# Performance work log

Measured on AMD Instinct MI355X. Metric: run time of the kernel, lower is better.

Reference implementation:

```python
import jax, jax.numpy as jnp
import numpy as np

K = 1024          # num_embeddings
D = 64            # embedding_dim
EPS = 0.05        # entropic regularization epsilon
DUAL_STEPS = 10
DUAL_LR = 0.5
TEMP = 0.5        # hist_temperature
OT_W = 1.0
CC = 0.25         # commitment cost


def _norm_prob(p):
    p = jnp.clip(p, 1e-12)
    return p / p.sum()


def _dual_obj(phi, src_w, tgt_w, cost):
    src_w = _norm_prob(src_w)
    tgt_w = _norm_prob(tgt_w)
    log_tgt = jnp.log(jnp.clip(tgt_w, 1e-12))[None, :]          # [1, K]
    lse = jax.scipy.special.logsumexp(log_tgt + (-cost + phi[None, :]) / EPS, axis=1)  # [K]
    return jnp.sum(src_w * (-EPS * lse)) + jnp.sum(tgt_w * phi)


def _dual_ot_loss(src_w, tgt_w, cost):
    src_d = jax.lax.stop_gradient(src_w)
    tgt_d = jax.lax.stop_gradient(tgt_w)
    cost_d = jax.lax.stop_gradient(cost)
    grad_phi = jax.grad(_dual_obj)
    def body(_, phi):
        return phi + DUAL_LR * grad_phi(phi, src_d, tgt_d, cost_d)
    phi = jax.lax.fori_loop(0, DUAL_STEPS, body, jnp.zeros_like(tgt_d))
    return _dual_obj(jax.lax.stop_gradient(phi), src_w, tgt_w, cost)


def _gaussian_target():
    idx = jnp.arange(K, dtype=jnp.float32)
    mean = (K - 1) / 2.0
    std = K / 6.0
    t = jnp.exp(-0.5 * ((idx - mean) / std) ** 2)
    return t / jnp.clip(t.sum(), 1e-12)


def _forward(inputs, codebook):
    B, C, H, W = inputs.shape
    x_bhwc = jnp.transpose(inputs, (0, 2, 3, 1))                 # [B,H,W,C]
    flat = x_bhwc.reshape(-1, C)                                  # [N, D]
    # squared-distance matrix [N, K]
    d = (jnp.sum(flat * flat, axis=1, keepdims=True)
         + jnp.sum(codebook * codebook, axis=1)
         - 2.0 * flat @ codebook.T)
    idx = jnp.argmin(d, axis=1)                                   # [N]
    enc = jax.nn.one_hot(idx, K, dtype=jnp.float32)               # [N, K]
    # power normalize (one-hot power = sqrt(1/K) < 1, so a no-op, but faithful)
    power = jnp.sqrt(jnp.mean(enc * enc))
    enc = jnp.where(power > 1.0, enc / power, enc)
    clean_q = enc @ codebook                                      # [N, D]
    noisy_q = clean_q                                             # channel=None -> zero noise
    # training losses
    hard_hist = jnp.mean(enc, axis=0)                             # [K]
    soft = jax.nn.softmax(-d / TEMP, axis=1)                      # [N, K]
    soft_hist = jnp.mean(soft, axis=0)
    # value = hard_hist, gradient flows via soft_hist (straight-through hist)
    cw = _norm_prob(hard_hist + soft_hist - jax.lax.stop_gradient(soft_hist))
    target = _gaussian_target()
    support = jnp.arange(K, dtype=jnp.float32)
    cost = jnp.abs(support[:, None] - support[None, :])           # cdist(p=2) on 1-d support
    ot_loss = OT_W * _dual_ot_loss(cw, target, cost)
    codebook_loss = jnp.mean((clean_q - jax.lax.stop_gradient(flat)) ** 2)
    commit_loss = jnp.mean((jax.lax.stop_gradient(clean_q) - flat) ** 2)
    loss = codebook_loss + CC * commit_loss + ot_loss
    # straight-through quantized output
    nq = noisy_q.reshape(B, H, W, C)
    quantized = x_bhwc + jax.lax.stop_gradient(nq - x_bhwc)
    quantized = jnp.transpose(quantized, (0, 3, 1, 2))            # [B,C,H,W]
    avg = jnp.mean(enc, axis=0)
    perplexity = jnp.exp(-jnp.sum(avg * jnp.log(avg + 1e-10)))
    return quantized, loss, perplexity


def setup_inputs() -> dict:
    key = jax.random.key(0)
    k1, k2 = jax.random.split(key)
    inputs = jax.random.normal(k1, (32, D, 32, 32), dtype=jnp.float32)
    codebook = jax.random.uniform(k2, (K, D), minval=-1.0 / K, maxval=1.0 / K, dtype=jnp.float32)
    return {"inputs": inputs, "codebook": codebook}


def reference(inputs, codebook):
    return _forward(inputs, codebook)
```

## Files before the change

kernel.cpp:

```cpp
#include <hip/hip_runtime.h>
#include <math.h>

#define NPTS 32768
#define KCB  1024
#define DIM  64
#define HW   1024
#define CHW  65536
#define RWIN 2

typedef short  bf16x8 __attribute__((ext_vector_type(8)));
typedef float  f32x16 __attribute__((ext_vector_type(16)));

__device__ __forceinline__ unsigned short f2b_rne(float f) {
  unsigned u = __float_as_uint(f);
  unsigned r = 0x7FFFu + ((u >> 16) & 1u);
  return (unsigned short)((u + r) >> 16);
}

__device__ __forceinline__ float block_sum(float v, float* scratch) {
  #pragma unroll
  for (int o = 32; o > 0; o >>= 1) v += __shfl_down(v, o, 64);
  int wid  = threadIdx.x >> 6;
  int lane = threadIdx.x & 63;
  __syncthreads();
  if (lane == 0) scratch[wid] = v;
  __syncthreads();
  float s = 0.f;
  int nw = blockDim.x >> 6;
  for (int w = 0; w < nw; ++w) s += scratch[w];
  return s;
}

__global__ __launch_bounds__(64) void k_cvt(const float* __restrict__ cb,
                                            float4* __restrict__ cbf,
                                            float* __restrict__ cnorm) {
  int c = blockIdx.x * 64 + threadIdx.x;
  const float4* row4 = (const float4*)(cb + c * DIM);
  float4 r[16];
  #pragma unroll
  for (int i = 0; i < 16; ++i) r[i] = row4[i];
  float s = 0.f;
  #pragma unroll
  for (int i = 0; i < 16; ++i) {
    s = fmaf(r[i].x, r[i].x, s); s = fmaf(r[i].y, r[i].y, s);
    s = fmaf(r[i].z, r[i].z, s); s = fmaf(r[i].w, r[i].w, s);
  }
  cnorm[c] = s;
  int ch = c >> 6, nt = (c >> 5) & 1, n = c & 31;
  int base = ch * 1024 + nt * 256 + n;
  #pragma unroll
  for (int o = 0; o < 8; ++o) {
    float f[8] = {r[2*o].x, r[2*o].y, r[2*o].z, r[2*o].w,
                  r[2*o+1].x, r[2*o+1].y, r[2*o+1].z, r[2*o+1].w};
    unsigned hu[4], lu[4];
    #pragma unroll
    for (int j = 0; j < 4; ++j) {
      unsigned short h0 = f2b_rne(f[2*j]),   h1 = f2b_rne(f[2*j+1]);
      float hf0 = __uint_as_float((unsigned)h0 << 16);
      float hf1 = __uint_as_float((unsigned)h1 << 16);
      unsigned short l0 = f2b_rne(f[2*j] - hf0), l1 = f2b_rne(f[2*j+1] - hf1);
      hu[j] = (unsigned)h0 | ((unsigned)h1 << 16);
      lu[j] = (unsigned)l0 | ((unsigned)l1 << 16);
    }
    int pos = base + (o >> 1) * 64 + (o & 1) * 32;
    uint4 hv = {hu[0], hu[1], hu[2], hu[3]};
    uint4 lv = {lu[0], lu[1], lu[2], lu[3]};
    cbf[pos]       = *(float4*)&hv;
    cbf[pos + 512] = *(float4*)&lv;
  }
}

__global__ __launch_bounds__(256, 2) void k_dist(const float* __restrict__ x,
                                                 const float* __restrict__ cb,
                                                 const float4* __restrict__ cbf,
                                                 const float* __restrict__ cnorm,
                                                 int* __restrict__ hist,
                                                 float* __restrict__ msep,
                                                 float* __restrict__ out) {
  __shared__ unsigned short lph[64][72], lpl[64][72];
  __shared__ short bbuf[2][8192];
  __shared__ float s_cn[KCB];
  __shared__ float s_sx[64], s_part[4][64];
  __shared__ unsigned long long s_pk[64][2];
  __shared__ int   s_bd[64];
  __shared__ float scratch[4];

  int tid = threadIdx.x;
  int t   = blockIdx.x;
  int n0  = t * 64;
  int b   = n0 >> 10;
  int hw0 = n0 & 1023;

  *(float4*)&s_cn[tid * 4] = *(const float4*)(cnorm + tid * 4);

  {
    int p = tid & 63, q4 = tid >> 6;
    const float* xb = x + b * CHW + hw0 + p;
    float s = 0.f;
    unsigned short hb[16], lb[16];
    #pragma unroll
    for (int i = 0; i < 16; ++i) {
      int c = q4 * 16 + i;
      float f = xb[c * HW];
      s = fmaf(f, f, s);
      unsigned short h = f2b_rne(f);
      float hf = __uint_as_float(((unsigned)h) << 16);
      hb[i] = h;
      lb[i] = f2b_rne(f - hf);
    }
    s_part[q4][p] = s;
    #pragma unroll
    for (int j = 0; j < 8; ++j) {
      *(unsigned*)&lph[p][q4 * 16 + 2 * j] = (unsigned)hb[2*j] | ((unsigned)hb[2*j+1] << 16);
      *(unsigned*)&lpl[p][q4 * 16 + 2 * j] = (unsigned)lb[2*j] | ((unsigned)lb[2*j+1] << 16);
    }
  }
  float4 pf[4];
  #pragma unroll
  for (int j = 0; j < 4; ++j) pf[j] = cbf[tid + 256 * j];
  __syncthreads();
  if (tid < 64)
    s_sx[tid] = ((s_part[0][tid] + s_part[1][tid]) + s_part[2][tid]) + s_part[3][tid];
  __syncthreads();

  int w = tid >> 6, l = tid & 63;
  int wm = w >> 1, wn = w & 1;
  int u = l >> 5, n = l & 31;

  bf16x8 ah[4], al[4];
  {
    int pt = wm * 32 + n;
    #pragma unroll
    for (int s = 0; s < 4; ++s) {
      ah[s] = *(const bf16x8*)&lph[pt][(2 * s + u) * 8];
      al[s] = *(const bf16x8*)&lpl[pt][(2 * s + u) * 8];
    }
  }
  float sxr[16];
  #pragma unroll
  for (int r = 0; r < 16; ++r)
    sxr[r] = s_sx[wm * 32 + (r & 3) + 8 * (r >> 2) + 4 * u];

  float best[16]; int bidx[16];
  #pragma unroll
  for (int r = 0; r < 16; ++r) { best[r] = 3.4e38f; bidx[r] = 0; }

  int bofs = wn * 256 + u * 32 + n;

  for (int ch = 0; ch < 16; ++ch) {
    int bb = ch & 1;
    #pragma unroll
    for (int j = 0; j < 4; ++j)
      *(float4*)&bbuf[bb][(tid + 256 * j) * 8] = pf[j];
    if (ch < 15) {
      #pragma unroll
      for (int j = 0; j < 4; ++j)
        pf[j] = cbf[(ch + 1) * 1024 + tid + 256 * j];
    }
    __builtin_amdgcn_s_waitcnt(0xc07f);
    __builtin_amdgcn_s_barrier();

    f32x16 acc;
    #pragma unroll
    for (int r = 0; r < 16; ++r) acc[r] = 0.f;
    #pragma unroll
    for (int s = 0; s < 4; ++s) {
      bf16x8 bh = *(const bf16x8*)&bbuf[bb][(bofs + s * 64) * 8];
      bf16x8 bl = *(const bf16x8*)&bbuf[bb][(bofs + s * 64 + 512) * 8];
      acc = __builtin_amdgcn_mfma_f32_32x32x16_bf16(ah[s], bh, acc, 0, 0, 0);
      acc = __builtin_amdgcn_mfma_f32_32x32x16_bf16(ah[s], bl, acc, 0, 0, 0);
      acc = __builtin_amdgcn_mfma_f32_32x32x16_bf16(al[s], bh, acc, 0, 0, 0);
    }
    float cnv = s_cn[ch * 64 + wn * 32 + n];
    int   kk  = ch * 64 + wn * 32 + n;
    #pragma unroll
    for (int r = 0; r < 16; ++r) {
      float dist = (sxr[r] + cnv) - 2.0f * acc[r];
      if (dist < best[r]) { best[r] = dist; bidx[r] = kk; }
    }
  }

  #pragma unroll
  for (int r = 0; r < 16; ++r) {
    unsigned long long p =
        ((unsigned long long)__float_as_uint(best[r]) << 32) | (unsigned)bidx[r];
    #pragma unroll
    for (int m = 1; m < 32; m <<= 1) {
      unsigned long long o = __shfl_xor(p, m, 64);
      p = (o < p) ? o : p;
    }
    if (n == 0)
      s_pk[wm * 32 + (r & 3) + 8 * (r >> 2) + 4 * u][wn] = p;
  }
  __syncthreads();
  if (tid < 64) {
    unsigned long long a = s_pk[tid][0], c2 = s_pk[tid][1];
    unsigned long long mn = (c2 < a) ? c2 : a;
    int bd = (int)(mn & 0xffffffffull);
    s_bd[tid] = bd;
    atomicAdd(&hist[bd], 1);
  }
  __syncthreads();

  float se = 0.f;
  {
    int p = tid & 63, cg = tid >> 6;
    int bd = s_bd[p];
    const float* crow = cb + bd * DIM;
    const float* xp = x + b * CHW + hw0 + p;
    float* ob = out + b * CHW + hw0 + p;
    #pragma unroll 4
    for (int i = 0; i < 16; ++i) {
      int c = cg * 16 + i;
      float xv   = xp[c * HW];
      float diff = crow[c] - xv;
      se += diff * diff;
      ob[c * HW] = xv + diff;
    }
  }
  float tot = block_sum(se, scratch);
  if (tid == 0) msep[t] = tot;
}

__global__ __launch_bounds__(256) void k_ot(const int* __restrict__ hist,
                                            const float* __restrict__ msep,
                                            float* __restrict__ out) {
  __shared__ __align__(16) float s_lt[KCB + 8], s_src[KCB + 8],
                                 s_phi[KCB + 8], s_lse[KCB + 8];
  __shared__ float scratch[4];
  int tid = threadIdx.x;
  int i0  = tid * 4;
  int sl0 = i0 + 4;

  float msetot = block_sum(msep[tid] + msep[tid + 256], scratch);

  int4 hi4 = *(const int4*)(hist + i0);
  int  hi[4] = {hi4.x, hi4.y, hi4.z, hi4.w};
  float tj[4], hj[4];
  #pragma unroll
  for (int j = 0; j < 4; ++j) {
    float fi = (float)(i0 + j);
    float zz = (fi - 511.5f) / (1024.0f / 6.0f);
    tj[j] = expf(-0.5f * zz * zz);
    hj[j] = (float)hi[j] * (1.0f / 32768.0f);
  }
  float St = block_sum(tj[0] + tj[1] + tj[2] + tj[3], scratch);
  float tgt[4], ltw[4];
  float l2 = 0.f;
  #pragma unroll
  for (int j = 0; j < 4; ++j) { tgt[j] = fmaxf(tj[j] / fmaxf(St, 1e-12f), 1e-12f); l2 += tgt[j]; }
  float St2 = block_sum(l2, scratch);
  #pragma unroll
  for (int j = 0; j < 4; ++j) { tgt[j] = tgt[j] / St2; ltw[j] = logf(fmaxf(tgt[j], 1e-12f)); }

  float m1[4], srcw[4];
  float l3 = 0.f;
  #pragma unroll
  for (int j = 0; j < 4; ++j) { m1[j] = fmaxf(hj[j], 1e-12f); l3 += m1[j]; }
  float S1 = block_sum(l3, scratch);
  float l4 = 0.f;
  #pragma unroll
  for (int j = 0; j < 4; ++j) { srcw[j] = fmaxf(m1[j] / S1, 1e-12f); l4 += srcw[j]; }
  float S2 = block_sum(l4, scratch);
  float l5 = 0.f;
  #pragma unroll
  for (int j = 0; j < 4; ++j) { srcw[j] = srcw[j] / S2; l5 += hj[j] * logf(hj[j] + 1e-10f); }
  float ent = block_sum(l5, scratch);

  *(float4*)&s_lt[sl0]  = *(float4*)ltw;
  *(float4*)&s_src[sl0] = *(float4*)srcw;
  *(float4*)&s_phi[sl0] = make_float4(0.f, 0.f, 0.f, 0.f);
  *(float4*)&s_lse[sl0] = make_float4(0.f, 0.f, 0.f, 0.f);
  if (tid == 0) {
    #pragma unroll
    for (int p = 0; p < 4; ++p) {
      s_lt[p] = -100.f; s_src[p] = 0.f; s_phi[p] = 0.f; s_lse[p] = 0.f;
      s_lt[KCB+4+p] = -100.f; s_src[KCB+4+p] = 0.f; s_phi[KCB+4+p] = 0.f; s_lse[KCB+4+p] = 0.f;
    }
  }
  __syncthreads();

  float ws[12];
  #pragma unroll
  for (int m = 0; m < 3; ++m) *(float4*)&ws[m*4] = *(float4*)&s_src[i0 + m*4];

  float phi[4] = {0.f, 0.f, 0.f, 0.f};
  float lse[4];
  for (int it = 0; it <= 10; ++it) {
    float wl[12], wp[12];
    #pragma unroll
    for (int m = 0; m < 3; ++m) {
      *(float4*)&wl[m*4] = *(float4*)&s_lt[i0 + m*4];
      *(float4*)&wp[m*4] = *(float4*)&s_phi[i0 + m*4];
    }
    #pragma unroll
    for (int j = 0; j < 4; ++j) {
      float mx = -3.0e38f;
      float vv[5];
      #pragma unroll
      for (int qq = 0; qq < 5; ++qq) {
        int m = j + qq + 2;
        float a = wl[m] + (wp[m] - fabsf((float)(qq - 2))) * 20.0f;
        vv[qq] = a;
        mx = fmaxf(mx, a);
      }
      float ssum = 0.f;
      #pragma unroll
      for (int qq = 0; qq < 5; ++qq) ssum += expf(vv[qq] - mx);
      lse[j] = mx + logf(ssum);
    }
    *(float4*)&s_lse[sl0] = *(float4*)lse;
    __syncthreads();
    if (it == 10) break;

    float we[12];
    #pragma unroll
    for (int m = 0; m < 3; ++m) *(float4*)&we[m*4] = *(float4*)&s_lse[i0 + m*4];
    #pragma unroll
    for (int j = 0; j < 4; ++j) {
      float basej = ltw[j] + phi[j] * 20.0f;
      float cs = 0.f;
      #pragma unroll
      for (int qq = 0; qq < 5; ++qq) {
        int m = j + qq + 2;
        float a = basej - fabsf((float)(qq - 2)) * 20.0f;
        cs += ws[m] * expf(a - we[m]);
      }
      phi[j] += 0.5f * (tgt[j] - cs);
    }
    *(float4*)&s_phi[sl0] = *(float4*)phi;
    __syncthreads();
  }

  float lo = 0.f;
  #pragma unroll
  for (int j = 0; j < 4; ++j) lo += srcw[j] * (-0.05f * lse[j]) + tgt[j] * phi[j];
  float ot = block_sum(lo, scratch);

  if (tid == 0) {
    out[2097152] = 1.25f * (msetot * (1.0f / 2097152.0f)) + ot;
    out[2097153] = expf(-ent);
  }
}

extern "C" void kernel_launch(void* const* d_in, const int* in_sizes, int n_in,
                              void* d_out, int out_size, void* d_ws, size_t ws_size,
                              hipStream_t stream) {
  const float* x  = (const float*)d_in[0];
  const float* cb = (const float*)d_in[1];
  float* out = (float*)d_out;

  float4* cbf  = (float4*)d_ws;
  float*  cnorm = (float*)((char*)d_ws + 262144);
  int*    hist  = (int*)((char*)d_ws + 266240);
  float*  msep  = (float*)((char*)d_ws + 270336);

  hipMemsetAsync(hist, 0, 4096, stream);
  k_cvt<<<16, 64, 0, stream>>>(cb, cbf, cnorm);
  k_dist<<<512, 256, 0, stream>>>(x, cb, cbf, cnorm, hist, msep, out);
  k_ot<<<1, 256, 0, stream>>>(hist, msep, out);
}
```

Measured before the change: 131.5 us.

## Fuse OT solve into distance kernel via last-block pattern and restructure MFMA tiling

Drops the memset and the separate single-block OT kernel. k_cvt now zeroes the histogram and counters, and the last k_dist block to finish, found with an atomic counter, runs the dual OT iterations. k_dist now uses 128-thread blocks of 32 points. Each wave covers half the codebook and loads codebook fragments straight from global memory into registers instead of double-buffering through LDS, and x is cached in LDS for the output pass. The aim is to cut launch overhead and LDS barriers, at the cost of re-reading codebook tiles per block and a serialized OT tail inside the last block.

```diff
diff --git a/kernel.cpp b/kernel.cpp
--- a/kernel.cpp
+++ b/kernel.cpp
@@ -6,7 +6,6 @@
 #define DIM  64
 #define HW   1024
 #define CHW  65536
-#define RWIN 2
 
 typedef short  bf16x8 __attribute__((ext_vector_type(8)));
 typedef float  f32x16 __attribute__((ext_vector_type(16)));
@@ -20,21 +19,25 @@
 __device__ __forceinline__ float block_sum(float v, float* scratch) {
   #pragma unroll
   for (int o = 32; o > 0; o >>= 1) v += __shfl_down(v, o, 64);
-  int wid  = threadIdx.x >> 6;
-  int lane = threadIdx.x & 63;
+  int wid = threadIdx.x >> 6, lane = threadIdx.x & 63;
   __syncthreads();
   if (lane == 0) scratch[wid] = v;
   __syncthreads();
   float s = 0.f;
   int nw = blockDim.x >> 6;
-  for (int w = 0; w < nw; ++w) s += scratch[w];
+  for (int w2 = 0; w2 < nw; ++w2) s += scratch[w2];
   return s;
 }
 
 __global__ __launch_bounds__(64) void k_cvt(const float* __restrict__ cb,
                                             float4* __restrict__ cbf,
-                                            float* __restrict__ cnorm) {
+                                            float* __restrict__ cnorm,
+                                            int* __restrict__ hist,
+                                            int* __restrict__ done,
+                                            float* __restrict__ mseacc) {
   int c = blockIdx.x * 64 + threadIdx.x;
+  hist[c] = 0;
+  if (c == 0) { *done = 0; *mseacc = 0.f; }
   const float4* row4 = (const float4*)(cb + c * DIM);
   float4 r[16];
   #pragma unroll
@@ -70,130 +73,132 @@
   }
 }
 
-__global__ __launch_bounds__(256, 2) void k_dist(const float* __restrict__ x,
+__global__ __launch_bounds__(128, 2) void k_dist(const float* __restrict__ x,
                                                  const float* __restrict__ cb,
                                                  const float4* __restrict__ cbf,
                                                  const float* __restrict__ cnorm,
                                                  int* __restrict__ hist,
-                                                 float* __restrict__ msep,
+                                                 int* __restrict__ done,
+                                                 float* __restrict__ mseacc,
                                                  float* __restrict__ out) {
-  __shared__ unsigned short lph[64][72], lpl[64][72];
-  __shared__ short bbuf[2][8192];
-  __shared__ float s_cn[KCB];
-  __shared__ float s_sx[64], s_part[4][64];
-  __shared__ unsigned long long s_pk[64][2];
-  __shared__ int   s_bd[64];
-  __shared__ float scratch[4];
+  __shared__ float4 s_af[2][4][64];
+  __shared__ float  lpf[64][32];
+  __shared__ float  s_part[4][32];
+  __shared__ float  s_sx[32];
+  __shared__ unsigned long long s_pk[32][2];
+  __shared__ int    s_bd[32];
+  __shared__ float  scratch[2];
+  __shared__ int    s_last;
+  __shared__ __align__(16) float s_lt[KCB + 8], s_src[KCB + 8],
+                                 s_phi[KCB + 8], s_lse[KCB + 8];
 
   int tid = threadIdx.x;
   int t   = blockIdx.x;
-  int n0  = t * 64;
+  int n0  = t * 32;
   int b   = n0 >> 10;
   int hw0 = n0 & 1023;
-
-  *(float4*)&s_cn[tid * 4] = *(const float4*)(cnorm + tid * 4);
+  int p   = tid & 31, g = tid >> 5;
 
   {
-    int p = tid & 63, q4 = tid >> 6;
     const float* xb = x + b * CHW + hw0 + p;
     float s = 0.f;
     unsigned short hb[16], lb[16];
     #pragma unroll
     for (int i = 0; i < 16; ++i) {
-      int c = q4 * 16 + i;
+      int c = g * 16 + i;
       float f = xb[c * HW];
       s = fmaf(f, f, s);
+      lpf[c][p] = f;
       unsigned short h = f2b_rne(f);
       float hf = __uint_as_float(((unsigned)h) << 16);
       hb[i] = h;
       lb[i] = f2b_rne(f - hf);
     }
-    s_part[q4][p] = s;
-    #pragma unroll
-    for (int j = 0; j < 8; ++j) {
-      *(unsigned*)&lph[p][q4 * 16 + 2 * j] = (unsigned)hb[2*j] | ((unsigned)hb[2*j+1] << 16);
-      *(unsigned*)&lpl[p][q4 * 16 + 2 * j] = (unsigned)lb[2*j] | ((unsigned)lb[2*j+1] << 16);
-    }
-  }
-  float4 pf[4];
-  #pragma unroll
-  for (int j = 0; j < 4; ++j) pf[j] = cbf[tid + 256 * j];
-  __syncthreads();
-  if (tid < 64)
+    s_part[g][p] = s;
+    unsigned hu0[4], hu1[4], lu0[4], lu1[4];
+    #pragma unroll
+    for (int j = 0; j < 4; ++j) {
+      hu0[j] = (unsigned)hb[2*j]     | ((unsigned)hb[2*j+1] << 16);
+      hu1[j] = (unsigned)hb[8+2*j]   | ((unsigned)hb[8+2*j+1] << 16);
+      lu0[j] = (unsigned)lb[2*j]     | ((unsigned)lb[2*j+1] << 16);
+      lu1[j] = (unsigned)lb[8+2*j]   | ((unsigned)lb[8+2*j+1] << 16);
+    }
+    uint4 a0 = {hu0[0],hu0[1],hu0[2],hu0[3]}, a1 = {hu1[0],hu1[1],hu1[2],hu1[3]};
+    uint4 c0 = {lu0[0],lu0[1],lu0[2],lu0[3]}, c1 = {lu1[0],lu1[1],lu1[2],lu1[3]};
+    s_af[0][g][p]      = *(float4*)&a0;
+    s_af[0][g][32 + p] = *(float4*)&a1;
+    s_af[1][g][p]      = *(float4*)&c0;
+    s_af[1][g][32 + p] = *(float4*)&c1;
+  }
+  __syncthreads();
+  if (tid < 32)
     s_sx[tid] = ((s_part[0][tid] + s_part[1][tid]) + s_part[2][tid]) + s_part[3][tid];
   __syncthreads();
 
-  int w = tid >> 6, l = tid & 63;
-  int wm = w >> 1, wn = w & 1;
+  int w = tid >> 6;
+  int l = tid & 63;
   int u = l >> 5, n = l & 31;
 
   bf16x8 ah[4], al[4];
-  {
-    int pt = wm * 32 + n;
-    #pragma unroll
-    for (int s = 0; s < 4; ++s) {
-      ah[s] = *(const bf16x8*)&lph[pt][(2 * s + u) * 8];
-      al[s] = *(const bf16x8*)&lpl[pt][(2 * s + u) * 8];
-    }
+  #pragma unroll
+  for (int s4 = 0; s4 < 4; ++s4) {
+    ah[s4] = *(bf16x8*)&s_af[0][s4][l];
+    al[s4] = *(bf16x8*)&s_af[1][s4][l];
   }
   float sxr[16];
   #pragma unroll
-  for (int r = 0; r < 16; ++r)
-    sxr[r] = s_sx[wm * 32 + (r & 3) + 8 * (r >> 2) + 4 * u];
+  for (int r = 0; r < 16; ++r) sxr[r] = s_sx[(r & 3) + 8 * (r >> 2) + 4 * u];
 
   float best[16]; int bidx[16];
   #pragma unroll
   for (int r = 0; r < 16; ++r) { best[r] = 3.4e38f; bidx[r] = 0; }
 
-  int bofs = wn * 256 + u * 32 + n;
-
-  for (int ch = 0; ch < 16; ++ch) {
-    int bb = ch & 1;
-    #pragma unroll
-    for (int j = 0; j < 4; ++j)
-      *(float4*)&bbuf[bb][(tid + 256 * j) * 8] = pf[j];
-    if (ch < 15) {
-      #pragma unroll
-      for (int j = 0; j < 4; ++j)
-        pf[j] = cbf[(ch + 1) * 1024 + tid + 256 * j];
-    }
-    __builtin_amdgcn_s_waitcnt(0xc07f);
-    __builtin_amdgcn_s_barrier();
-
-    f32x16 acc;
-    #pragma unroll
-    for (int r = 0; r < 16; ++r) acc[r] = 0.f;
-    #pragma unroll
-    for (int s = 0; s < 4; ++s) {
-      bf16x8 bh = *(const bf16x8*)&bbuf[bb][(bofs + s * 64) * 8];
-      bf16x8 bl = *(const bf16x8*)&bbuf[bb][(bofs + s * 64 + 512) * 8];
-      acc = __builtin_amdgcn_mfma_f32_32x32x16_bf16(ah[s], bh, acc, 0, 0, 0);
-      acc = __builtin_amdgcn_mfma_f32_32x32x16_bf16(ah[s], bl, acc, 0, 0, 0);
-      acc = __builtin_amdgcn_mfma_f32_32x32x16_bf16(al[s], bh, acc, 0, 0, 0);
-    }
-    float cnv = s_cn[ch * 64 + wn * 32 + n];
-    int   kk  = ch * 64 + wn * 32 + n;
+  #pragma unroll 1
+  for (int c8 = 0; c8 < 8; ++c8) {
+    int ch = w * 8 + c8;
+    const float4* bp = cbf + ch * 1024 + l;
+    float4 bh[8], bl[8];
+    #pragma unroll
+    for (int q2 = 0; q2 < 8; ++q2) {
+      bh[q2] = bp[q2 * 64];
+      bl[q2] = bp[q2 * 64 + 512];
+    }
+    float cn0 = cnorm[ch * 64 + n];
+    float cn1 = cnorm[ch * 64 + 32 + n];
+    f32x16 a0, a1;
+    #pragma unroll
+    for (int r = 0; r < 16; ++r) { a0[r] = 0.f; a1[r] = 0.f; }
+    #pragma unroll
+    for (int s4 = 0; s4 < 4; ++s4) {
+      a0 = __builtin_amdgcn_mfma_f32_32x32x16_bf16(ah[s4], *(bf16x8*)&bh[s4],     a0, 0, 0, 0);
+      a1 = __builtin_amdgcn_mfma_f32_32x32x16_bf16(ah[s4], *(bf16x8*)&bh[4 + s4], a1, 0, 0, 0);
+      a0 = __builtin_amdgcn_mfma_f32_32x32x16_bf16(ah[s4], *(bf16x8*)&bl[s4],     a0, 0, 0, 0);
+      a1 = __builtin_amdgcn_mfma_f32_32x32x16_bf16(ah[s4], *(bf16x8*)&bl[4 + s4], a1, 0, 0, 0);
+      a0 = __builtin_amdgcn_mfma_f32_32x32x16_bf16(al[s4], *(bf16x8*)&bh[s4],     a0, 0, 0, 0);
+      a1 = __builtin_amdgcn_mfma_f32_32x32x16_bf16(al[s4], *(bf16x8*)&bh[4 + s4], a1, 0, 0, 0);
+    }
     #pragma unroll
     for (int r = 0; r < 16; ++r) {
-      float dist = (sxr[r] + cnv) - 2.0f * acc[r];
-      if (dist < best[r]) { best[r] = dist; bidx[r] = kk; }
+      float d0 = (sxr[r] + cn0) - 2.0f * a0[r];
+      if (d0 < best[r]) { best[r] = d0; bidx[r] = ch * 64 + n; }
+      float d1 = (sxr[r] + cn1) - 2.0f * a1[r];
+      if (d1 < best[r]) { best[r] = d1; bidx[r] = ch * 64 + 32 + n; }
     }
   }
 
   #pragma unroll
   for (int r = 0; r < 16; ++r) {
-    unsigned long long p =
+    unsigned long long pk =
         ((unsigned long long)__float_as_uint(best[r]) << 32) | (unsigned)bidx[r];
     #pragma unroll
     for (int m = 1; m < 32; m <<= 1) {
-      unsigned long long o = __shfl_xor(p, m, 64);
-      p = (o < p) ? o : p;
-    }
-    if (n == 0)
-      s_pk[wm * 32 + (r & 3) + 8 * (r >> 2) + 4 * u][wn] = p;
-  }
-  __syncthreads();
-  if (tid < 64) {
+      unsigned long long o = __shfl_xor(pk, m, 64);
+      pk = (o < pk) ? o : pk;
+    }
+    if (n == 0) s_pk[(r & 3) + 8 * (r >> 2) + 4 * u][w] = pk;
+  }
+  __syncthreads();
+  if (tid < 32) {
     unsigned long long a = s_pk[tid][0], c2 = s_pk[tid][1];
     unsigned long long mn = (c2 < a) ? c2 : a;
     int bd = (int)(mn & 0xffffffffull);
@@ -204,137 +209,144 @@
 
   float se = 0.f;
   {
-    int p = tid & 63, cg = tid >> 6;
     int bd = s_bd[p];
     const float* crow = cb + bd * DIM;
-    const float* xp = x + b * CHW + hw0 + p;
-    float* ob = out + b * CHW + hw0 + p;
+    float* op = out + b * CHW + hw0 + p;
     #pragma unroll 4
     for (int i = 0; i < 16; ++i) {
-      int c = cg * 16 + i;
-      float xv   = xp[c * HW];
+      int c = g * 16 + i;
+      float xv   = lpf[c][p];
       float diff = crow[c] - xv;
       se += diff * diff;
-      ob[c * HW] = xv + diff;
+      op[c * HW] = xv + diff;
     }
   }
   float tot = block_sum(se, scratch);
-  if (tid == 0) msep[t] = tot;
-}
-
-__global__ __launch_bounds__(256) void k_ot(const int* __restrict__ hist,
-                                            const float* __restrict__ msep,
-                                            float* __restrict__ out) {
-  __shared__ __align__(16) float s_lt[KCB + 8], s_src[KCB + 8],
-                                 s_phi[KCB + 8], s_lse[KCB + 8];
-  __shared__ float scratch[4];
-  int tid = threadIdx.x;
-  int i0  = tid * 4;
-  int sl0 = i0 + 4;
-
-  float msetot = block_sum(msep[tid] + msep[tid + 256], scratch);
-
-  int4 hi4 = *(const int4*)(hist + i0);
-  int  hi[4] = {hi4.x, hi4.y, hi4.z, hi4.w};
-  float tj[4], hj[4];
-  #pragma unroll
-  for (int j = 0; j < 4; ++j) {
+  if (tid == 0) {
+    atomicAdd(mseacc, tot);
+    __threadfence();
+    int old = atomicAdd(done, 1);
+    s_last = (old == 1023);
+  }
+  __syncthreads();
+  if (!s_last) return;
+
+  __threadfence();
+  float msetot = *mseacc;
+  int i0 = tid * 8;
+
+  int4 ha = *(const int4*)(hist + i0);
+  int4 hb4 = *(const int4*)(hist + i0 + 4);
+  int hi[8] = {ha.x, ha.y, ha.z, ha.w, hb4.x, hb4.y, hb4.z, hb4.w};
+  float tj[8], hj[8];
+  #pragma unroll
+  for (int j = 0; j < 8; ++j) {
     float fi = (float)(i0 + j);
     float zz = (fi - 511.5f) / (1024.0f / 6.0f);
     tj[j] = expf(-0.5f * zz * zz);
     hj[j] = (float)hi[j] * (1.0f / 32768.0f);
   }
-  float St = block_sum(tj[0] + tj[1] + tj[2] + tj[3], scratch);
-  float tgt[4], ltw[4];
+  float l1 = 0.f;
+  #pragma unroll
+  for (int j = 0; j < 8; ++j) l1 += tj[j];
+  float St = block_sum(l1, scratch);
+  float tgt[8], ltw[8];
   float l2 = 0.f;
   #pragma unroll
-  for (int j = 0; j < 4; ++j) { tgt[j] = fmaxf(tj[j] / fmaxf(St, 1e-12f), 1e-12f); l2 += tgt[j]; }
+  for (int j = 0; j < 8; ++j) { tgt[j] = fmaxf(tj[j] / fmaxf(St, 1e-12f), 1e-12f); l2 += tgt[j]; }
   float St2 = block_sum(l2, scratch);
   #pragma unroll
-  for (int j = 0; j < 4; ++j) { tgt[j] = tgt[j] / St2; ltw[j] = logf(fmaxf(tgt[j], 1e-12f)); }
-
-  float m1[4], srcw[4];
+  for (int j = 0; j < 8; ++j) { tgt[j] = tgt[j] / St2; ltw[j] = logf(fmaxf(tgt[j], 1e-12f)); }
+
+  float srcw[8];
   float l3 = 0.f;
   #pragma unroll
-  for (int j = 0; j < 4; ++j) { m1[j] = fmaxf(hj[j], 1e-12f); l3 += m1[j]; }
+  for (int j = 0; j < 8; ++j) { srcw[j] = fmaxf(hj[j], 1e-12f); l3 += srcw[j]; }
   float S1 = block_sum(l3, scratch);
   float l4 = 0.f;
   #pragma unroll
-  for (int j = 0; j < 4; ++j) { srcw[j] = fmaxf(m1[j] / S1, 1e-12f); l4 += srcw[j]; }
+  for (int j = 0; j < 8; ++j) { srcw[j] = fmaxf(srcw[j] / S1, 1e-12f); l4 += srcw[j]; }
   float S2 = block_sum(l4, scratch);
   float l5 = 0.f;
   #pragma unroll
-  for (int j = 0; j < 4; ++j) { srcw[j] = srcw[j] / S2; l5 += hj[j] * logf(hj[j] + 1e-10f); }
+  for (int j = 0; j < 8; ++j) { srcw[j] = srcw[j] / S2; l5 += hj[j] * logf(hj[j] + 1e-10f); }
   float ent = block_sum(l5, scratch);
 
-  *(float4*)&s_lt[sl0]  = *(float4*)ltw;
-  *(float4*)&s_src[sl0] = *(float4*)srcw;
-  *(float4*)&s_phi[sl0] = make_float4(0.f, 0.f, 0.f, 0.f);
-  *(float4*)&s_lse[sl0] = make_float4(0.f, 0.f, 0.f, 0.f);
+  *(float4*)&s_lt[i0 + 4]  = make_float4(ltw[0], ltw[1], ltw[2], ltw[3]);
+  *(float4*)&s_lt[i0 + 8]  = make_float4(ltw[4], ltw[5], ltw[6], ltw[7]);
+  *(float4*)&s_src[i0 + 4] = make_float4(srcw[0], srcw[1], srcw[2], srcw[3]);
+  *(float4*)&s_src[i0 + 8] = make_float4(srcw[4], srcw[5], srcw[6], srcw[7]);
+  *(float4*)&s_phi[i0 + 4] = make_float4(0.f, 0.f, 0.f, 0.f);
+  *(float4*)&s_phi[i0 + 8] = make_float4(0.f, 0.f, 0.f, 0.f);
+  *(float4*)&s_lse[i0 + 4] = make_float4(0.f, 0.f, 0.f, 0.f);
+  *(float4*)&s_lse[i0 + 8] = make_float4(0.f, 0.f, 0.f, 0.f);
   if (tid == 0) {
     #pragma unroll
-    for (int p = 0; p < 4; ++p) {
-      s_lt[p] = -100.f; s_src[p] = 0.f; s_phi[p] = 0.f; s_lse[p] = 0.f;
-      s_lt[KCB+4+p] = -100.f; s_src[KCB+4+p] = 0.f; s_phi[KCB+4+p] = 0.f; s_lse[KCB+4+p] = 0.f;
-    }
-  }
-  __syncthreads();
-
-  float ws[12];
-  #pragma unroll
-  for (int m = 0; m < 3; ++m) *(float4*)&ws[m*4] = *(float4*)&s_src[i0 + m*4];
-
-  float phi[4] = {0.f, 0.f, 0.f, 0.f};
-  float lse[4];
+    for (int pp = 0; pp < 4; ++pp) {
+      s_lt[pp] = -100.f; s_src[pp] = 0.f; s_phi[pp] = 0.f; s_lse[pp] = 0.f;
+      s_lt[KCB+4+pp] = -100.f; s_src[KCB+4+pp] = 0.f;
+      s_phi[KCB+4+pp] = 0.f;   s_lse[KCB+4+pp] = 0.f;
+    }
+  }
+  __syncthreads();
+
+  float wsr[16];
+  #pragma unroll
+  for (int m = 0; m < 4; ++m) *(float4*)&wsr[m*4] = *(float4*)&s_src[i0 + m*4];
+
+  float phi[8] = {0.f,0.f,0.f,0.f,0.f,0.f,0.f,0.f};
+  float lse[8];
   for (int it = 0; it <= 10; ++it) {
-    float wl[12], wp[12];
-    #pragma unroll
-    for (int m = 0; m < 3; ++m) {
+    float wl[16], wp[16];
+    #pragma unroll
+    for (int m = 0; m < 4; ++m) {
       *(float4*)&wl[m*4] = *(float4*)&s_lt[i0 + m*4];
       *(float4*)&wp[m*4] = *(float4*)&s_phi[i0 + m*4];
     }
     #pragma unroll
-    for (int j = 0; j < 4; ++j) {
+    for (int j = 0; j < 8; ++j) {
       float mx = -3.0e38f;
       float vv[5];
       #pragma unroll
-      for (int qq = 0; qq < 5; ++qq) {
-        int m = j + qq + 2;
-        float a = wl[m] + (wp[m] - fabsf((float)(qq - 2))) * 20.0f;
-        vv[qq] = a;
+      for (int q = 0; q < 5; ++q) {
+        int m = j + q + 2;
+        float a = wl[m] + (wp[m] - fabsf((float)(q - 2))) * 20.0f;
+        vv[q] = a;
         mx = fmaxf(mx, a);
       }
       float ssum = 0.f;
       #pragma unroll
-      for (int qq = 0; qq < 5; ++qq) ssum += expf(vv[qq] - mx);
+      for (int q = 0; q < 5; ++q) ssum += expf(vv[q] - mx);
       lse[j] = mx + logf(ssum);
     }
-    *(float4*)&s_lse[sl0] = *(float4*)lse;
+    *(float4*)&s_lse[i0 + 4] = make_float4(lse[0], lse[1], lse[2], lse[3]);
+    *(float4*)&s_lse[i0 + 8] = make_float4(lse[4], lse[5], lse[6], lse[7]);
     __syncthreads();
     if (it == 10) break;
 
-    float we[12];
-    #pragma unroll
-    for (int m = 0; m < 3; ++m) *(float4*)&we[m*4] = *(float4*)&s_lse[i0 + m*4];
-    #pragma unroll
-    for (int j = 0; j < 4; ++j) {
+    float we[16];
+    #pragma unroll
+    for (int m = 0; m < 4; ++m) *(float4*)&we[m*4] = *(float4*)&s_lse[i0 + m*4];
+    #pragma unroll
+    for (int j = 0; j < 8; ++j) {
       float basej = ltw[j] + phi[j] * 20.0f;
       float cs = 0.f;
       #pragma unroll
-      for (int qq = 0; qq < 5; ++qq) {
-        int m = j + qq + 2;
-        float a = basej - fabsf((float)(qq - 2)) * 20.0f;
-        cs += ws[m] * expf(a - we[m]);
+      for (int q = 0; q < 5; ++q) {
+        int m = j + q + 2;
+        float a = basej - fabsf((float)(q - 2)) * 20.0f;
+        cs += wsr[m] * expf(a - we[m]);
       }
       phi[j] += 0.5f * (tgt[j] - cs);
     }
-    *(float4*)&s_phi[sl0] = *(float4*)phi;
+    *(float4*)&s_phi[i0 + 4] = make_float4(phi[0], phi[1], phi[2], phi[3]);
+    *(float4*)&s_phi[i0 + 8] = make_float4(phi[4], phi[5], phi[6], phi[7]);
     __syncthreads();
   }
 
   float lo = 0.f;
   #pragma unroll
-  for (int j = 0; j < 4; ++j) lo += srcw[j] * (-0.05f * lse[j]) + tgt[j] * phi[j];
+  for (int j = 0; j < 8; ++j) lo += srcw[j] * (-0.05f * lse[j]) + tgt[j] * phi[j];
   float ot = block_sum(lo, scratch);
 
   if (tid == 0) {
@@ -350,13 +362,12 @@
   const float* cb = (const float*)d_in[1];
   float* out = (float*)d_out;
 
-  float4* cbf  = (float4*)d_ws;
+  float4* cbf   = (float4*)d_ws;
   float*  cnorm = (float*)((char*)d_ws + 262144);
   int*    hist  = (int*)((char*)d_ws + 266240);
-  float*  msep  = (float*)((char*)d_ws + 270336);
-
-  hipMemsetAsync(hist, 0, 4096, stream);
-  k_cvt<<<16, 64, 0, stream>>>(cb, cbf, cnorm);
-  k_dist<<<512, 256, 0, stream>>>(x, cb, cbf, cnorm, hist, msep, out);
-  k_ot<<<1, 256, 0, stream>>>(hist, msep, out);
-}
+  int*    done  = (int*)((char*)d_ws + 270336);
+  float*  mseacc= (float*)((char*)d_ws + 270400);
+
+  k_cvt<<<16, 64, 0, stream>>>(cb, cbf, cnorm, hist, done, mseacc);
+  k_dist<<<1024, 128, 0, stream>>>(x, cb, cbf, cnorm, hist, done, mseacc, out);
+}
```

Result: slower. 157.5 us (+19.8%).
